# Optimization experiments

Hardware: AMD Instinct MI355X
Metric: run time of the kernel (lower is better)

The kernel has to match this reference:

```python
import jax, jax.numpy as jnp
import numpy as np

NV, NF, NM = 8192, 4096, 12288
PREFIX, DOM = 3, 16
IN_CH, OUT_CH = 64, 64
EMB = IN_CH - PREFIX  # 61
N = NV + NF + 2 * NM  # 36864
E = 262144
G, K = 8192, 16
NUM_COLOR = 100
ATT_HEADS = 4


def setup_inputs() -> dict:
    rng = np.random.default_rng(0)
    key = jax.random.key(0)
    def nrm(i, shape, s=0.1):
        return jax.random.normal(jax.random.fold_in(key, i), shape, jnp.float32) * s
    edge_index = jnp.asarray(rng.integers(0, N, (2, E)), jnp.int32)
    vn_colors = jnp.asarray(rng.integers(0, NUM_COLOR, (NV,)), jnp.int32)
    # ragged neighbor structure: per group, full src list (target included once)
    tgt = rng.integers(0, NF, G)
    deg = rng.integers(1, K + 1, G)
    full = rng.integers(0, NF, (G, K))
    full = np.where(full == tgt[:, None], (tgt[:, None] + 1) % NF, full)
    full[np.arange(G), rng.integers(0, deg)] = tgt
    mask = np.arange(K)[None, :] < deg[:, None]
    mult = rng.integers(1, 6, G)  # (len(target) - 1) in original
    return dict(
        edge_index=edge_index, vn_colors=vn_colors,
        group_full=jnp.asarray(full, jnp.int32), group_mask=jnp.asarray(mask),
        group_tgt=jnp.asarray(tgt, jnp.int32), group_mult=jnp.asarray(mult, jnp.int32),
        vn_prefix=nrm(0, (NV, PREFIX)), fn_embed=nrm(1, (NF, IN_CH)),
        v2f_msgs=nrm(2, (NM, DOM)), v2f_hidden=nrm(3, (NM, EMB)),
        f2v_msgs=nrm(4, (NM, DOM)), f2v_hidden=nrm(5, (NM, EMB)),
        msg_prefix=nrm(6, (2 * NM, PREFIX)),
        emb=nrm(7, (NUM_COLOR, EMB)),
        gru_v2f_wih=nrm(8, (3 * EMB, DOM)), gru_v2f_whh=nrm(9, (3 * EMB, EMB)),
        gru_v2f_bih=nrm(10, (3 * EMB,)), gru_v2f_bhh=nrm(11, (3 * EMB,)),
        gru_f2v_wih=nrm(12, (3 * EMB, DOM)), gru_f2v_whh=nrm(13, (3 * EMB, EMB)),
        gru_f2v_bih=nrm(14, (3 * EMB,)), gru_f2v_bhh=nrm(15, (3 * EMB,)),
        W1=nrm(16, (IN_CH, 32)), a1s=nrm(17, (4, 8)), a1d=nrm(18, (4, 8)), b1=nrm(19, (32,)),
        W2=nrm(20, (32, 32)), a2s=nrm(21, (4, 8)), a2d=nrm(22, (4, 8)), b2=nrm(23, (32,)),
        W3=nrm(24, (32, 32)), a3s=nrm(25, (4, 8)), a3d=nrm(26, (4, 8)), b3=nrm(27, (32,)),
        W4=nrm(28, (32, 4 * OUT_CH)), a4s=nrm(29, (4, OUT_CH)), a4d=nrm(30, (4, OUT_CH)), b4=nrm(31, (OUT_CH,)),
        att_wq=nrm(32, (ATT_HEADS, OUT_CH, OUT_CH)), att_wk=nrm(33, (ATT_HEADS, OUT_CH, OUT_CH)),
        att_ws=nrm(34, (ATT_HEADS, 2 * OUT_CH)), att_b=nrm(35, (ATT_HEADS,)),
    )


def _gru(x, h, w_ih, w_hh, b_ih, b_hh):
    gi = x @ w_ih.T + b_ih
    gh = h @ w_hh.T + b_hh
    hsz = h.shape[1]
    r = jax.nn.sigmoid(gi[:, :hsz] + gh[:, :hsz])
    z = jax.nn.sigmoid(gi[:, hsz:2 * hsz] + gh[:, hsz:2 * hsz])
    n = jnp.tanh(gi[:, 2 * hsz:] + r * gh[:, 2 * hsz:])
    return (1.0 - z) * n + z * h


def _gat(x, src, dst, W, a_src, a_dst, bias, heads, ch, concat):
    n = x.shape[0]
    xl = (x @ W).reshape(n, heads, ch)          # [N,H,C]
    a_s = (xl * a_src).sum(-1)                  # [N,H]
    a_d = (xl * a_dst).sum(-1)
    e = jax.nn.leaky_relu(a_s[src] + a_d[dst], 0.2)   # [E',H]
    m = jax.ops.segment_max(e, dst, num_segments=n)
    ex = jnp.exp(e - m[dst])
    den = jax.ops.segment_sum(ex, dst, num_segments=n)
    alpha = ex / den[dst]
    out = jax.ops.segment_sum(alpha[:, :, None] * xl[src], dst, num_segments=n)
    out = out.reshape(n, heads * ch) if concat else out.mean(axis=1)
    return out + bias


def _forward(floats, edge_index, vn_colors, group_full, group_mask, group_tgt, group_mult):
    (vn_prefix, fn_embed, v2f_msgs, v2f_hidden, f2v_msgs, f2v_hidden, msg_prefix, emb,
     gv_wih, gv_whh, gv_bih, gv_bhh, gf_wih, gf_whh, gf_bih, gf_bhh,
     W1, a1s, a1d, b1, W2, a2s, a2d, b2, W3, a3s, a3d, b3, W4, a4s, a4d, b4,
     att_wq, att_wk, att_ws, att_b) = floats
    x_v = jnp.concatenate([vn_prefix, emb[vn_colors]], axis=1)    # [NV, IN_CH]
    v2f_h = _gru(v2f_msgs, v2f_hidden, gv_wih, gv_whh, gv_bih, gv_bhh)
    f2v_h = _gru(f2v_msgs, f2v_hidden, gf_wih, gf_whh, gf_bih, gf_bhh)
    hid = jnp.concatenate([msg_prefix, jnp.concatenate([v2f_h, f2v_h], axis=0)], axis=1)
    x = jnp.concatenate([x_v, fn_embed, hid], axis=0)             # [N, IN_CH]
    loop = jnp.arange(x.shape[0], dtype=edge_index.dtype)         # self-loops (PyG default)
    src = jnp.concatenate([edge_index[0], loop])
    dst = jnp.concatenate([edge_index[1], loop])
    x = jax.nn.leaky_relu(_gat(x, src, dst, W1, a1s, a1d, b1, 4, 8, True), 0.01)
    x = jax.nn.leaky_relu(_gat(x, src, dst, W2, a2s, a2d, b2, 4, 8, True), 0.01)
    x = jax.nn.leaky_relu(_gat(x, src, dst, W3, a3s, a3d, b3, 4, 8, True), 0.01)
    x = jax.nn.leaky_relu(_gat(x, src, dst, W4, a4s, a4d, b4, 4, OUT_CH, False), 0.01)
    pool = x[NV:NV + NF]                                          # [NF, OUT_CH]
    # attention_scores[q*NF + k, h] = sigmoid(q_proj(pool[q]).Wsq + k_proj(pool[k]).Wsk + b)
    qs = jnp.einsum('nd,hde,he->nh', pool, att_wq, att_ws[:, :OUT_CH])
    ks = jnp.einsum('nd,hde,he->nh', pool, att_wk, att_ws[:, OUT_CH:])
    S = jax.nn.sigmoid(qs[:, None, :] + ks[None, :, :] + att_b)   # [NF, NF, H]
    t = group_tgt
    scores = S[t[:, None], group_full]                            # [G,K,H]
    is_tgt = (group_full == t[:, None]) & group_mask
    nbr = group_mask & (~is_tgt)
    nm = nbr[:, :, None]
    degm1 = nbr.sum(-1)                                           # neighbors excl. target
    score_sum = jnp.where(nm, scores, 0.0).sum(axis=1) / jnp.maximum(degm1, 1)[:, None]
    trg_score = S[t, t]                                           # [G,H]
    mx = jnp.maximum(score_sum, trg_score)
    e0 = jnp.exp(score_sum - mx)
    e1 = jnp.exp(trg_score - mx)
    tw0 = e0 / (e0 + e1)
    tw1 = e1 / (e0 + e1)
    w = jax.nn.softmax(jnp.where(nm, scores, -1e30), axis=1)      # segment softmax over nbrs
    w = w * tw0[:, None, :] * group_mult[:, None, None].astype(w.dtype)
    out = jnp.where(is_tgt[:, :, None], tw1[:, None, :], jnp.where(nm, w, 0.0))
    out = jnp.where((degm1 == 0)[:, None, None], 0.0, out)        # single-src groups -> zeros
    return out, v2f_h, f2v_h


def reference(edge_index, vn_colors, group_full, group_mask, group_tgt, group_mult,
              vn_prefix, fn_embed, v2f_msgs, v2f_hidden, f2v_msgs, f2v_hidden, msg_prefix,
              emb, gru_v2f_wih, gru_v2f_whh, gru_v2f_bih, gru_v2f_bhh,
              gru_f2v_wih, gru_f2v_whh, gru_f2v_bih, gru_f2v_bhh,
              W1, a1s, a1d, b1, W2, a2s, a2d, b2, W3, a3s, a3d, b3, W4, a4s, a4d, b4,
              att_wq, att_wk, att_ws, att_b):
    floats = (vn_prefix, fn_embed, v2f_msgs, v2f_hidden, f2v_msgs, f2v_hidden, msg_prefix,
              emb, gru_v2f_wih, gru_v2f_whh, gru_v2f_bih, gru_v2f_bhh,
              gru_f2v_wih, gru_f2v_whh, gru_f2v_bih, gru_f2v_bhh,
              W1, a1s, a1d, b1, W2, a2s, a2d, b2, W3, a3s, a3d, b3, W4, a4s, a4d, b4,
              att_wq, att_wk, att_ws, att_b)
    return _forward(floats, edge_index, vn_colors, group_full, group_mask, group_tgt, group_mult)
```

## Files before the change

### kernel.cpp

```cpp
#include <hip/hip_runtime.h>
#include <hip/hip_bf16.h>

#define NV 8192
#define NF 4096
#define NM 12288
#define PFX 3
#define DOM 16
#define EMB 61
#define NN 36864
#define EE 262144
#define GG 8192
#define KK 16
#define OUT0 524288

typedef __hip_bfloat16 bf16;
__device__ __forceinline__ float b2f(bf16 x) { return __bfloat162float(x); }
__device__ __forceinline__ float lrelu(float x, float s) { return x > 0.f ? x : s * x; }
__device__ __forceinline__ float sigm(float x) { return 1.f / (1.f + expf(-x)); }
__device__ __forceinline__ float LD(const void* p, int i, int f) {
  return f ? ((const float*)p)[i] : b2f(((const bf16*)p)[i]);
}
__device__ __forceinline__ void ST(void* p, int i, int f, float v) {
  if (f) ((float*)p)[i] = v; else ((bf16*)p)[i] = __float2bfloat16(v);
}
__device__ __forceinline__ int MK(const void* p, int i, int bytey) {
  return bytey ? (int)((const signed char*)p)[i] : ((const int*)p)[i];
}

__global__ void k_detect(const void* fn, const void* mask, int* flags) {
  if (threadIdx.x || blockIdx.x) return;
  int wild = 0;
  const bf16* h = (const bf16*)fn;
  for (int i = 0; i < 128; ++i) {
    float x = b2f(h[i]);
    float a = fabsf(x);
    if (a != a || a > 1e4f || (x != 0.f && a < 1e-8f)) ++wild;
  }
  flags[0] = (wild >= 8) ? 1 : 0;
  const int* mi = (const int*)mask;
  int bytey = 0;
  for (int i = 0; i < 64; ++i) {
    unsigned v = (unsigned)mi[i];
    if (v > 1u) bytey = 1;
  }
  flags[1] = bytey;
}

__global__ void k_precomp(const void* gv_wih, const void* gv_whh,
                          const void* gf_wih, const void* gf_whh,
                          const void* W4, const void* a4s, const void* a4d,
                          const void* wq, const void* wk, const void* ws,
                          float* Wt, float* waS, float* waD, float* wqv, float* wkv,
                          const int* flg) {
  int f = flg[0];
  int blk = blockIdx.x, tid = threadIdx.x;
  if (blk < 116) {
    int t = blk * 256 + tid;
    if (t < 2 * 77 * 192) {
      int dir = t / (77 * 192);
      int rem = t - dir * 77 * 192;
      int d = rem / 192, o = rem - d * 192;
      const void* wih = dir ? gf_wih : gv_wih;
      const void* whh = dir ? gf_whh : gv_whh;
      float v = 0.f;
      if (o < 183) v = (d < 16) ? LD(wih, o * 16 + d, f) : LD(whh, o * 61 + (d - 16), f);
      Wt[t] = v;
    }
  } else if (blk == 116) {
    int isD = tid >= 128;
    int u = tid & 127;
    int h = u >> 5, k = u & 31;
    const void* av = isD ? a4d : a4s;
    float acc = 0.f;
    for (int c = 0; c < 64; ++c) acc += LD(W4, k * 256 + h * 64 + c, f) * LD(av, h * 64 + c, f);
    (isD ? waD : waS)[h * 32 + k] = acc;
  } else {
    int h = tid >> 6, d = tid & 63;
    float q = 0.f, k = 0.f;
    for (int e = 0; e < 64; ++e) {
      q += LD(wq, h * 4096 + d * 64 + e, f) * LD(ws, h * 128 + e, f);
      k += LD(wk, h * 4096 + d * 64 + e, f) * LD(ws, h * 128 + 64 + e, f);
    }
    wqv[h * 64 + d] = q;
    wkv[h * 64 + d] = k;
  }
}

__global__ __launch_bounds__(256) void k_gru2(
    const void* v2f_msgs, const void* v2f_hid, const void* f2v_msgs, const void* f2v_hid,
    const void* gv_bih, const void* gv_bhh, const void* gf_bih, const void* gf_bhh,
    const float* Wt, float* hidcat, void* outv, const int* flg) {
  int f = flg[0];
  int blk = blockIdx.x;
  int dir = blk >= 384;
  int loc = dir ? blk - 384 : blk;
  int gr0 = loc * 32;
  const void* msgs = dir ? f2v_msgs : v2f_msgs;
  const void* hid = dir ? f2v_hid : v2f_hid;
  const void* bih = dir ? gf_bih : gv_bih;
  const void* bhh = dir ? gf_bhh : gv_bhh;
  const float* W = Wt + dir * 77 * 192;

  __shared__ float smem[7808];
  float* F = smem;
  float* G1 = smem;
  float* G2 = smem + 32 * 183;

  int tid = threadIdx.x;
  for (int idx = tid; idx < 32 * 16; idx += 256) {
    int r = idx >> 4, d = idx & 15;
    F[d * 36 + r] = LD(msgs, (gr0 + r) * DOM + d, f);
  }
  for (int idx = tid; idx < 32 * 61; idx += 256) {
    int r = idx / 61, d = idx - r * 61;
    F[(16 + d) * 36 + r] = LD(hid, gr0 * 61 + idx, f);
  }
  __syncthreads();

  int og = tid & 15, rg = tid >> 4;
  int o0 = og * 12, r0 = rg * 2;
  float accA[24], accB[24];
#pragma unroll
  for (int i = 0; i < 24; ++i) { accA[i] = 0.f; accB[i] = 0.f; }

#pragma unroll 2
  for (int d = 0; d < 16; ++d) {
    const float2 fv2 = *(const float2*)&F[d * 36 + r0];
    const float4 w0 = *(const float4*)&W[d * 192 + o0];
    const float4 w1 = *(const float4*)&W[d * 192 + o0 + 4];
    const float4 w2 = *(const float4*)&W[d * 192 + o0 + 8];
    float wv[12] = {w0.x, w0.y, w0.z, w0.w, w1.x, w1.y, w1.z, w1.w, w2.x, w2.y, w2.z, w2.w};
#pragma unroll
    for (int k = 0; k < 12; ++k) {
      accA[k * 2 + 0] += wv[k] * fv2.x;
      accA[k * 2 + 1] += wv[k] * fv2.y;
    }
  }
#pragma unroll 2
  for (int d = 16; d < 77; ++d) {
    const float2 fv2 = *(const float2*)&F[d * 36 + r0];
    const float4 w0 = *(const float4*)&W[d * 192 + o0];
    const float4 w1 = *(const float4*)&W[d * 192 + o0 + 4];
    const float4 w2 = *(const float4*)&W[d * 192 + o0 + 8];
    float wv[12] = {w0.x, w0.y, w0.z, w0.w, w1.x, w1.y, w1.z, w1.w, w2.x, w2.y, w2.z, w2.w};
#pragma unroll
    for (int k = 0; k < 12; ++k) {
      accB[k * 2 + 0] += wv[k] * fv2.x;
      accB[k * 2 + 1] += wv[k] * fv2.y;
    }
  }
  __syncthreads();

#pragma unroll
  for (int k = 0; k < 12; ++k) {
    int o = o0 + k;
    if (o < 183) {
      float biv = LD(bih, o, f), bhv = LD(bhh, o, f);
#pragma unroll
      for (int m = 0; m < 2; ++m) {
        int r = r0 + m;
        float gi = accA[k * 2 + m] + biv;
        float gh = accB[k * 2 + m] + bhv;
        if (o < 122) G1[r * 183 + o] = gi + gh;
        else { G1[r * 183 + o] = gi; G2[r * 61 + (o - 122)] = gh; }
      }
    }
  }
  __syncthreads();

  int j = tid & 63, rq = tid >> 6;
  if (j < 61) {
    for (int rr = 0; rr < 8; ++rr) {
      int r = rq * 8 + rr;
      float gr = sigm(G1[r * 183 + j]);
      float gz = sigm(G1[r * 183 + 61 + j]);
      float gn = tanhf(G1[r * 183 + 122 + j] + gr * G2[r * 61 + j]);
      float hold = LD(hid, (gr0 + r) * 61 + j, f);
      float hn = (1.f - gz) * gn + gz * hold;
      int b = dir * NM + gr0 + r;
      hidcat[b * 61 + j] = hn;
      ST(outv, OUT0 + b * 61 + j, f, hn);
    }
  }
}

__global__ void k_deg(const int* dst, int* deg) {
  int e = blockIdx.x * blockDim.x + threadIdx.x;
  if (e < EE) atomicAdd(&deg[dst[e]], 1);
}
__global__ void k_scan1(const int* deg, int* rowptr, int* bsum) {
  __shared__ int s[512];
  int g = blockIdx.x * 512 + threadIdx.x;
  int v = (g < NN) ? deg[g] : 0;
  s[threadIdx.x] = v;
  __syncthreads();
  for (int off = 1; off < 512; off <<= 1) {
    int t = (threadIdx.x >= off) ? s[threadIdx.x - off] : 0;
    __syncthreads();
    s[threadIdx.x] += t;
    __syncthreads();
  }
  if (g < NN) rowptr[g] = s[threadIdx.x] - v;
  if (threadIdx.x == 511) bsum[blockIdx.x] = s[511];
}
__global__ void k_scan2(const int* bsum, int* boff, int nb) {
  __shared__ int s[128];
  int v = (threadIdx.x < nb) ? bsum[threadIdx.x] : 0;
  s[threadIdx.x] = v;
  __syncthreads();
  for (int off = 1; off < 128; off <<= 1) {
    int t = (threadIdx.x >= off) ? s[threadIdx.x - off] : 0;
    __syncthreads();
    s[threadIdx.x] += t;
    __syncthreads();
  }
  if (threadIdx.x < nb) boff[threadIdx.x] = s[threadIdx.x] - v;
}
__global__ void k_scan3(int* rowptr, const int* boff) {
  int g = blockIdx.x * blockDim.x + threadIdx.x;
  if (g < NN) rowptr[g] += boff[g >> 9];
  if (g == 0) rowptr[NN] = EE;
}
__global__ void k_fill(const int* src, const int* dst, const int* rowptr, int* cnt, int* col) {
  int e = blockIdx.x * blockDim.x + threadIdx.x;
  if (e < EE) {
    int d = dst[e];
    int pos = rowptr[d] + atomicAdd(&cnt[d], 1);
    col[pos] = src[e];
  }
}

__global__ __launch_bounds__(256) void k_xl1(
    const void* vn_prefix, const int* vn_colors, const void* emb, const void* fn_embed,
    const void* msg_prefix, const float* hidcat, const void* W1, const void* a1s,
    const void* a1d, float* xl, float* a_s, float* a_d, const int* flg) {
  int f = flg[0];
  __shared__ float Wl[64 * 32];
  __shared__ float X[8][64];
  int tid = threadIdx.x;
  for (int t = tid; t < 2048; t += 256) Wl[t] = LD(W1, t, f);
  for (int t = tid; t < 512; t += 256) {
    int r = t >> 6, c = t & 63;
    int i = blockIdx.x * 8 + r;
    float v;
    if (i < NV) {
      v = (c < PFX) ? LD(vn_prefix, i * PFX + c, f) : LD(emb, vn_colors[i] * EMB + (c - PFX), f);
    } else if (i < NV + NF) {
      v = LD(fn_embed, (size_t)(i - NV) * 64 + c, f);
    } else {
      int jj = i - NV - NF;
      v = (c < PFX) ? LD(msg_prefix, jj * PFX + c, f) : hidcat[jj * EMB + (c - PFX)];
    }
    X[r][c] = v;
  }
  __syncthreads();
  int j = tid & 31, r = tid >> 5;
  int i = blockIdx.x * 8 + r;
  float acc = 0.f;
#pragma unroll
  for (int k = 0; k < 64; ++k) acc += X[r][k] * Wl[k * 32 + j];
  xl[(size_t)i * 32 + j] = acc;
  float sw = LD(a1s, j, f), dw = LD(a1d, j, f);
  float p = acc * sw, q = acc * dw;
#pragma unroll
  for (int off = 1; off < 8; off <<= 1) {
    p += __shfl_xor(p, off);
    q += __shfl_xor(q, off);
  }
  if ((j & 7) == 0) {
    a_s[(size_t)i * 4 + (j >> 3)] = p;
    a_d[(size_t)i * 4 + (j >> 3)] = q;
  }
}

template <int MODE>
__global__ __launch_bounds__(256) void k_gather13(
    const int* rowptr, const int* col, const float* a_s, const float* a_d,
    const float* xl, const void* bias,
    const void* Wn, const void* asn_, const void* adn_,
    const float* waS, const float* waD,
    float* xl_next, float* xout, float* as_out, float* ad_out, const int* flg) {
  int f = flg[0];
  __shared__ int colb[16][64];
  __shared__ float4 eb[16][64];
  __shared__ float Wn_l[32 * 32];
  __shared__ float an_s[32], an_d[32];
  __shared__ float Xr[16][33];
  __shared__ float SwaS[128], SwaD[128];
  int tid = threadIdx.x;
  if (MODE == 0) {
    for (int t = tid; t < 1024; t += 256) Wn_l[t] = LD(Wn, t, f);
    if (tid < 32) { an_s[tid] = LD(asn_, tid, f); an_d[tid] = LD(adn_, tid, f); }
  } else {
    if (tid < 128) { SwaS[tid] = waS[tid]; SwaD[tid] = waD[tid]; }
  }
  int g = tid >> 4, l = tid & 15;
  int i = blockIdx.x * 16 + g;
  int beg = rowptr[i], end = rowptr[i + 1];
  int deg = end - beg;
  float4 adv = *(const float4*)(a_d + (size_t)i * 4);
  float4 asv = *(const float4*)(a_s + (size_t)i * 4);
  float ad[4] = {adv.x, adv.y, adv.z, adv.w};
  float es[4], mx[4];
  {
    float asl[4] = {asv.x, asv.y, asv.z, asv.w};
#pragma unroll
    for (int h = 0; h < 4; ++h) { es[h] = lrelu(asl[h] + ad[h], 0.2f); mx[h] = es[h]; }
  }
  float den[4] = {0.f, 0.f, 0.f, 0.f};
  int c0 = l, c1 = l + 16;
  int h0 = l >> 3, h1 = 2 + (l >> 3);
  float acc0, acc1;

  if (deg <= 64) {
    for (int s = l; s < deg; s += 16) {
      int j = col[beg + s];
      colb[g][s] = j;
      float4 aj = *(const float4*)(a_s + (size_t)j * 4);
      float e0 = lrelu(aj.x + ad[0], 0.2f);
      float e1 = lrelu(aj.y + ad[1], 0.2f);
      float e2 = lrelu(aj.z + ad[2], 0.2f);
      float e3 = lrelu(aj.w + ad[3], 0.2f);
      eb[g][s] = make_float4(e0, e1, e2, e3);
      mx[0] = fmaxf(mx[0], e0); mx[1] = fmaxf(mx[1], e1);
      mx[2] = fmaxf(mx[2], e2); mx[3] = fmaxf(mx[3], e3);
    }
#pragma unroll
    for (int off = 1; off < 16; off <<= 1)
#pragma unroll
      for (int h = 0; h < 4; ++h) mx[h] = fmaxf(mx[h], __shfl_xor(mx[h], off));
    for (int s = l; s < deg; s += 16) {
      float4 e4 = eb[g][s];
      float x0 = expf(e4.x - mx[0]), x1 = expf(e4.y - mx[1]);
      float x2 = expf(e4.z - mx[2]), x3 = expf(e4.w - mx[3]);
      eb[g][s] = make_float4(x0, x1, x2, x3);
      den[0] += x0; den[1] += x1; den[2] += x2; den[3] += x3;
    }
#pragma unroll
    for (int off = 1; off < 16; off <<= 1)
#pragma unroll
      for (int h = 0; h < 4; ++h) den[h] += __shfl_xor(den[h], off);
    float exS[4];
#pragma unroll
    for (int h = 0; h < 4; ++h) { exS[h] = expf(es[h] - mx[h]); den[h] += exS[h]; }
    acc0 = exS[h0] * xl[(size_t)i * 32 + c0];
    acc1 = exS[h1] * xl[(size_t)i * 32 + c1];
    for (int s = 0; s < deg; ++s) {
      int j = colb[g][s];
      float4 e4 = eb[g][s];
      float w0 = h0 ? e4.y : e4.x;
      float w1 = (l >> 3) ? e4.w : e4.z;
      acc0 += w0 * xl[(size_t)j * 32 + c0];
      acc1 += w1 * xl[(size_t)j * 32 + c1];
    }
  } else {
    for (int s = l; s < deg; s += 16) {
      int j = col[beg + s];
      float4 aj = *(const float4*)(a_s + (size_t)j * 4);
      mx[0] = fmaxf(mx[0], lrelu(aj.x + ad[0], 0.2f));
      mx[1] = fmaxf(mx[1], lrelu(aj.y + ad[1], 0.2f));
      mx[2] = fmaxf(mx[2], lrelu(aj.z + ad[2], 0.2f));
      mx[3] = fmaxf(mx[3], lrelu(aj.w + ad[3], 0.2f));
    }
#pragma unroll
    for (int off = 1; off < 16; off <<= 1)
#pragma unroll
      for (int h = 0; h < 4; ++h) mx[h] = fmaxf(mx[h], __shfl_xor(mx[h], off));
    for (int s = l; s < deg; s += 16) {
      int j = col[beg + s];
      float4 aj = *(const float4*)(a_s + (size_t)j * 4);
      den[0] += expf(lrelu(aj.x + ad[0], 0.2f) - mx[0]);
      den[1] += expf(lrelu(aj.y + ad[1], 0.2f) - mx[1]);
      den[2] += expf(lrelu(aj.z + ad[2], 0.2f) - mx[2]);
      den[3] += expf(lrelu(aj.w + ad[3], 0.2f) - mx[3]);
    }
#pragma unroll
    for (int off = 1; off < 16; off <<= 1)
#pragma unroll
      for (int h = 0; h < 4; ++h) den[h] += __shfl_xor(den[h], off);
    float exS[4];
#pragma unroll
    for (int h = 0; h < 4; ++h) { exS[h] = expf(es[h] - mx[h]); den[h] += exS[h]; }
    acc0 = exS[h0] * xl[(size_t)i * 32 + c0];
    acc1 = exS[h1] * xl[(size_t)i * 32 + c1];
    for (int s = 0; s < deg; ++s) {
      int j = col[beg + s];
      float e0 = lrelu(a_s[(size_t)j * 4 + h0] + ad[h0], 0.2f);
      float e1 = lrelu(a_s[(size_t)j * 4 + h1] + ad[h1], 0.2f);
      acc0 += expf(e0 - mx[h0]) * xl[(size_t)j * 32 + c0];
      acc1 += expf(e1 - mx[h1]) * xl[(size_t)j * 32 + c1];
    }
  }
  float v0 = lrelu(acc0 / den[h0] + LD(bias, c0, f), 0.01f);
  float v1 = lrelu(acc1 / den[h1] + LD(bias, c1, f), 0.01f);

  if (MODE == 0) {
    Xr[g][c0] = v0;
    Xr[g][c1] = v1;
    __syncthreads();
    float n0 = 0.f, n1 = 0.f;
#pragma unroll
    for (int k = 0; k < 32; ++k) {
      float xv = Xr[g][k];
      n0 += xv * Wn_l[k * 32 + c0];
      n1 += xv * Wn_l[k * 32 + c1];
    }
    xl_next[(size_t)i * 32 + c0] = n0;
    xl_next[(size_t)i * 32 + c1] = n1;
    float p0 = n0 * an_s[c0], q0 = n0 * an_d[c0];
    float p1 = n1 * an_s[c1], q1 = n1 * an_d[c1];
#pragma unroll
    for (int off = 1; off < 8; off <<= 1) {
      p0 += __shfl_xor(p0, off); q0 += __shfl_xor(q0, off);
      p1 += __shfl_xor(p1, off); q1 += __shfl_xor(q1, off);
    }
    if ((l & 7) == 0) {
      as_out[(size_t)i * 4 + h0] = p0;
      ad_out[(size_t)i * 4 + h0] = q0;
      as_out[(size_t)i * 4 + h1] = p1;
      ad_out[(size_t)i * 4 + h1] = q1;
    }
  } else {
    xout[(size_t)i * 32 + c0] = v0;
    xout[(size_t)i * 32 + c1] = v1;
    float pS[4], pD[4];
#pragma unroll
    for (int h = 0; h < 4; ++h) {
      pS[h] = v0 * SwaS[h * 32 + c0] + v1 * SwaS[h * 32 + c1];
      pD[h] = v0 * SwaD[h * 32 + c0] + v1 * SwaD[h * 32 + c1];
    }
#pragma unroll
    for (int off = 1; off < 16; off <<= 1)
#pragma unroll
      for (int h = 0; h < 4; ++h) { pS[h] += __shfl_xor(pS[h], off); pD[h] += __shfl_xor(pD[h], off); }
    if (l == 0) {
#pragma unroll
      for (int h = 0; h < 4; ++h) {
        as_out[(size_t)i * 4 + h] = pS[h];
        ad_out[(size_t)i * 4 + h] = pD[h];
      }
    }
  }
}

__global__ __launch_bounds__(256) void k_gather4(const int* rowptr, const int* col,
                                                 const float* a_s, const float* a_d,
                                                 const float* x, float* agg) {
  __shared__ int colb[16][64];
  __shared__ float4 eb[16][64];
  int tid = threadIdx.x;
  int g = tid >> 4, l = tid & 15;
  int i = NV + blockIdx.x * 16 + g;
  int beg = rowptr[i], end = rowptr[i + 1];
  int deg = end - beg;
  float4 adv = *(const float4*)(a_d + (size_t)i * 4);
  float4 asv = *(const float4*)(a_s + (size_t)i * 4);
  float ad[4] = {adv.x, adv.y, adv.z, adv.w};
  float es[4], mx[4];
  {
    float asl[4] = {asv.x, asv.y, asv.z, asv.w};
#pragma unroll
    for (int h = 0; h < 4; ++h) { es[h] = lrelu(asl[h] + ad[h], 0.2f); mx[h] = es[h]; }
  }
  float den[4] = {0.f, 0.f, 0.f, 0.f};
  int k0 = l, k1 = l + 16;
  float acc[4][2];

  if (deg <= 64) {
    for (int s = l; s < deg; s += 16) {
      int j = col[beg + s];
      colb[g][s] = j;
      float4 aj = *(const float4*)(a_s + (size_t)j * 4);
      float e0 = lrelu(aj.x + ad[0], 0.2f);
      float e1 = lrelu(aj.y + ad[1], 0.2f);
      float e2 = lrelu(aj.z + ad[2], 0.2f);
      float e3 = lrelu(aj.w + ad[3], 0.2f);
      eb[g][s] = make_float4(e0, e1, e2, e3);
      mx[0] = fmaxf(mx[0], e0); mx[1] = fmaxf(mx[1], e1);
      mx[2] = fmaxf(mx[2], e2); mx[3] = fmaxf(mx[3], e3);
    }
#pragma unroll
    for (int off = 1; off < 16; off <<= 1)
#pragma unroll
      for (int h = 0; h < 4; ++h) mx[h] = fmaxf(mx[h], __shfl_xor(mx[h], off));
    for (int s = l; s < deg; s += 16) {
      float4 e4 = eb[g][s];
      float x0 = expf(e4.x - mx[0]), x1 = expf(e4.y - mx[1]);
      float x2 = expf(e4.z - mx[2]), x3 = expf(e4.w - mx[3]);
      eb[g][s] = make_float4(x0, x1, x2, x3);
      den[0] += x0; den[1] += x1; den[2] += x2; den[3] += x3;
    }
#pragma unroll
    for (int off = 1; off < 16; off <<= 1)
#pragma unroll
      for (int h = 0; h < 4; ++h) den[h] += __shfl_xor(den[h], off);
    float exS[4];
#pragma unroll
    for (int h = 0; h < 4; ++h) { exS[h] = expf(es[h] - mx[h]); den[h] += exS[h]; }
    float xs0 = x[(size_t)i * 32 + k0], xs1 = x[(size_t)i * 32 + k1];
#pragma unroll
    for (int h = 0; h < 4; ++h) { acc[h][0] = exS[h] * xs0; acc[h][1] = exS[h] * xs1; }
    for (int s = 0; s < deg; ++s) {
      int j = colb[g][s];
      float4 e4 = eb[g][s];
      float xv0 = x[(size_t)j * 32 + k0], xv1 = x[(size_t)j * 32 + k1];
      acc[0][0] += e4.x * xv0; acc[0][1] += e4.x * xv1;
      acc[1][0] += e4.y * xv0; acc[1][1] += e4.y * xv1;
      acc[2][0] += e4.z * xv0; acc[2][1] += e4.z * xv1;
      acc[3][0] += e4.w * xv0; acc[3][1] += e4.w * xv1;
    }
  } else {
    for (int s = l; s < deg; s += 16) {
      int j = col[beg + s];
      float4 aj = *(const float4*)(a_s + (size_t)j * 4);
      mx[0] = fmaxf(mx[0], lrelu(aj.x + ad[0], 0.2f));
      mx[1] = fmaxf(mx[1], lrelu(aj.y + ad[1], 0.2f));
      mx[2] = fmaxf(mx[2], lrelu(aj.z + ad[2], 0.2f));
      mx[3] = fmaxf(mx[3], lrelu(aj.w + ad[3], 0.2f));
    }
#pragma unroll
    for (int off = 1; off < 16; off <<= 1)
#pragma unroll
      for (int h = 0; h < 4; ++h) mx[h] = fmaxf(mx[h], __shfl_xor(mx[h], off));
    for (int s = l; s < deg; s += 16) {
      int j = col[beg + s];
      float4 aj = *(const float4*)(a_s + (size_t)j * 4);
      den[0] += expf(lrelu(aj.x + ad[0], 0.2f) - mx[0]);
      den[1] += expf(lrelu(aj.y + ad[1], 0.2f) - mx[1]);
      den[2] += expf(lrelu(aj.z + ad[2], 0.2f) - mx[2]);
      den[3] += expf(lrelu(aj.w + ad[3], 0.2f) - mx[3]);
    }
#pragma unroll
    for (int off = 1; off < 16; off <<= 1)
#pragma unroll
      for (int h = 0; h < 4; ++h) den[h] += __shfl_xor(den[h], off);
    float exS[4];
#pragma unroll
    for (int h = 0; h < 4; ++h) { exS[h] = expf(es[h] - mx[h]); den[h] += exS[h]; }
    float xs0 = x[(size_t)i * 32 + k0], xs1 = x[(size_t)i * 32 + k1];
#pragma unroll
    for (int h = 0; h < 4; ++h) { acc[h][0] = exS[h] * xs0; acc[h][1] = exS[h] * xs1; }
    for (int s = 0; s < deg; ++s) {
      int j = col[beg + s];
      float4 aj = *(const float4*)(a_s + (size_t)j * 4);
      float xv0 = x[(size_t)j * 32 + k0], xv1 = x[(size_t)j * 32 + k1];
      acc[0][0] += expf(lrelu(aj.x + ad[0], 0.2f) - mx[0]) * xv0;
      acc[0][1] += expf(lrelu(aj.x + ad[0], 0.2f) - mx[0]) * xv1;
      acc[1][0] += expf(lrelu(aj.y + ad[1], 0.2f) - mx[1]) * xv0;
      acc[1][1] += expf(lrelu(aj.y + ad[1], 0.2f) - mx[1]) * xv1;
      acc[2][0] += expf(lrelu(aj.z + ad[2], 0.2f) - mx[2]) * xv0;
      acc[2][1] += expf(lrelu(aj.z + ad[2], 0.2f) - mx[2]) * xv1;
      acc[3][0] += expf(lrelu(aj.w + ad[3], 0.2f) - mx[3]) * xv0;
      acc[3][1] += expf(lrelu(aj.w + ad[3], 0.2f) - mx[3]) * xv1;
    }
  }
#pragma unroll
  for (int h = 0; h < 4; ++h) {
    agg[(size_t)i * 128 + h * 32 + k0] = acc[h][0] / den[h];
    agg[(size_t)i * 128 + h * 32 + k1] = acc[h][1] / den[h];
  }
}

__global__ __launch_bounds__(256) void k_l4_out(const float* agg, const void* W4, const void* b4,
                                                const float* wqv, const float* wkv,
                                                float* qs, float* ks, const int* flg) {
  int f = flg[0];
  __shared__ float Wl[128 * 64];
  __shared__ float Al[64][132];
  __shared__ float Ql[256], Kl[256];
  int tid = threadIdx.x;
  int R0 = NV + blockIdx.x * 64;
  for (int t = tid; t < 128 * 64; t += 256) {
    int K = t >> 6, c = t & 63;
    int h = K >> 5, k = K & 31;
    Wl[t] = LD(W4, k * 256 + h * 64 + c, f);
  }
  {
    const float4* ag4 = (const float4*)(agg + (size_t)R0 * 128);
    for (int t = tid; t < 2048; t += 256) {
      int r = t >> 5, k4 = (t & 31) << 2;
      float4 v = ag4[t];
      *(float4*)&Al[r][k4] = v;
    }
  }
  if (tid < 256) { Ql[tid] = wqv[tid]; Kl[tid] = wkv[tid]; }
  __syncthreads();
  int c0 = (tid & 15) << 2, r0 = (tid >> 4) << 2;
  float acc[4][4];
#pragma unroll
  for (int j = 0; j < 4; ++j)
#pragma unroll
    for (int i = 0; i < 4; ++i) acc[j][i] = 0.f;
#pragma unroll 4
  for (int K = 0; K < 128; ++K) {
    float4 wv = *(const float4*)&Wl[K * 64 + c0];
    float a0 = Al[r0][K], a1 = Al[r0 + 1][K], a2 = Al[r0 + 2][K], a3 = Al[r0 + 3][K];
    acc[0][0] += a0 * wv.x; acc[0][1] += a0 * wv.y; acc[0][2] += a0 * wv.z; acc[0][3] += a0 * wv.w;
    acc[1][0] += a1 * wv.x; acc[1][1] += a1 * wv.y; acc[1][2] += a1 * wv.z; acc[1][3] += a1 * wv.w;
    acc[2][0] += a2 * wv.x; acc[2][1] += a2 * wv.y; acc[2][2] += a2 * wv.z; acc[2][3] += a2 * wv.w;
    acc[3][0] += a3 * wv.x; acc[3][1] += a3 * wv.y; acc[3][2] += a3 * wv.z; acc[3][3] += a3 * wv.w;
  }
  float bv[4];
#pragma unroll
  for (int i = 0; i < 4; ++i) bv[i] = LD(b4, c0 + i, f);
  float o[4][4];
#pragma unroll
  for (int j = 0; j < 4; ++j)
#pragma unroll
    for (int i = 0; i < 4; ++i) o[j][i] = lrelu(0.25f * acc[j][i] + bv[i], 0.01f);
  int nbase = R0 - NV + r0;
#pragma unroll
  for (int j = 0; j < 4; ++j) {
#pragma unroll
    for (int h = 0; h < 4; ++h) {
      float pq = o[j][0] * Ql[h * 64 + c0] + o[j][1] * Ql[h * 64 + c0 + 1] +
                 o[j][2] * Ql[h * 64 + c0 + 2] + o[j][3] * Ql[h * 64 + c0 + 3];
      float pk = o[j][0] * Kl[h * 64 + c0] + o[j][1] * Kl[h * 64 + c0 + 1] +
                 o[j][2] * Kl[h * 64 + c0 + 2] + o[j][3] * Kl[h * 64 + c0 + 3];
#pragma unroll
      for (int off = 1; off < 16; off <<= 1) {
        pq += __shfl_xor(pq, off);
        pk += __shfl_xor(pk, off);
      }
      if ((tid & 15) == 0) {
        qs[(size_t)(nbase + j) * 4 + h] = pq;
        ks[(size_t)(nbase + j) * 4 + h] = pk;
      }
    }
  }
}

__global__ void k_groups(const int* full, const void* mask, const int* tgt, const int* mult,
                         const float* qs, const float* ks, const void* att_b, void* outv,
                         const int* flg) {
  int f = flg[0], mbyte = flg[1];
  int g = blockIdx.x;
  int lane = threadIdx.x;
  int k = lane >> 2, h = lane & 3;
  int t = tgt[g];
  int idx = full[g * KK + k];
  int mk = MK(mask, g * KK + k, mbyte);
  float bh = LD(att_b, h, f);
  float qt = qs[t * 4 + h];
  float sc = sigm(qt + ks[idx * 4 + h] + bh);
  int is_tgt = (idx == t) && mk;
  int nbr = mk && !is_tgt;
  unsigned long long bal = __ballot(nbr != 0);
  int degm1 = (int)(__popcll(bal) >> 2);
  float ssum = nbr ? sc : 0.f;
  for (int off = 4; off < 64; off <<= 1) ssum += __shfl_xor(ssum, off);
  ssum /= (float)(degm1 > 1 ? degm1 : 1);
  float trg = sigm(qt + ks[t * 4 + h] + bh);
  float mxv = fmaxf(ssum, trg);
  float e0 = expf(ssum - mxv), e1 = expf(trg - mxv);
  float tw0 = e0 / (e0 + e1), tw1 = e1 / (e0 + e1);
  float msc = nbr ? sc : -1e30f;
  float m = msc;
  for (int off = 4; off < 64; off <<= 1) m = fmaxf(m, __shfl_xor(m, off));
  float ex = expf(msc - m);
  float den = ex;
  for (int off = 4; off < 64; off <<= 1) den += __shfl_xor(den, off);
  float w = ex / den * tw0 * (float)mult[g];
  float res = is_tgt ? tw1 : (nbr ? w : 0.f);
  if (degm1 == 0) res = 0.f;
  ST(outv, g * 64 + k * 4 + h, f, res);
}

extern "C" void kernel_launch(void* const* d_in, const int* in_sizes, int n_in,
                              void* d_out, int out_size, void* d_ws, size_t ws_size,
                              hipStream_t stream) {
  const int* edge = (const int*)d_in[0];
  const int* esrc = edge;
  const int* edst = edge + EE;
  const int* vn_colors = (const int*)d_in[1];
  const int* group_full = (const int*)d_in[2];
  const void* group_mask = d_in[3];
  const int* group_tgt = (const int*)d_in[4];
  const int* group_mult = (const int*)d_in[5];
  const void* vn_prefix = d_in[6];
  const void* fn_embed = d_in[7];
  const void* v2f_msgs = d_in[8];
  const void* v2f_hidden = d_in[9];
  const void* f2v_msgs = d_in[10];
  const void* f2v_hidden = d_in[11];
  const void* msg_prefix = d_in[12];
  const void* emb = d_in[13];
  const void* gv_wih = d_in[14];
  const void* gv_whh = d_in[15];
  const void* gv_bih = d_in[16];
  const void* gv_bhh = d_in[17];
  const void* gf_wih = d_in[18];
  const void* gf_whh = d_in[19];
  const void* gf_bih = d_in[20];
  const void* gf_bhh = d_in[21];
  const void* W1 = d_in[22];
  const void* a1s = d_in[23];
  const void* a1d = d_in[24];
  const void* b1 = d_in[25];
  const void* W2 = d_in[26];
  const void* a2s = d_in[27];
  const void* a2d = d_in[28];
  const void* b2 = d_in[29];
  const void* W3 = d_in[30];
  const void* a3s = d_in[31];
  const void* a3d = d_in[32];
  const void* b3 = d_in[33];
  const void* W4 = d_in[34];
  const void* a4s = d_in[35];
  const void* a4d = d_in[36];
  const void* b4 = d_in[37];
  const void* att_wq = d_in[38];
  const void* att_wk = d_in[39];
  const void* att_ws = d_in[40];
  const void* att_b = d_in[41];

  char* w = (char*)d_ws;
  size_t off = 0;
  auto carve = [&](size_t bytes) -> void* {
    void* p = w + off;
    off += (bytes + 255) & ~(size_t)255;
    return p;
  };
  int* flags = (int*)carve(16);
  float* Wt = (float*)carve((size_t)2 * 77 * 192 * 4);
  float* hidcat = (float*)carve((size_t)2 * NM * EMB * 4);
  float* xB = (float*)carve((size_t)NN * 64 * 4);
  float* scr = (float*)carve((size_t)NN * 128 * 4);
  float* a_sA = (float*)carve((size_t)NN * 4 * 4);
  float* a_dA = (float*)carve((size_t)NN * 4 * 4);
  float* a_sB = (float*)carve((size_t)NN * 4 * 4);
  float* a_dB = (float*)carve((size_t)NN * 4 * 4);
  int* deg = (int*)carve((size_t)2 * NN * 4);
  int* cnt = deg + NN;
  int* rowptr = (int*)carve((size_t)(NN + 1) * 4);
  int* bsum = (int*)carve(128 * 4);
  int* boff = (int*)carve(128 * 4);
  int* col = (int*)carve((size_t)EE * 4);
  float* qs = (float*)carve((size_t)NF * 4 * 4);
  float* ks = (float*)carve((size_t)NF * 4 * 4);
  float* wqv = (float*)carve(256 * 4);
  float* wkv = (float*)carve(256 * 4);
  float* waS = (float*)carve(128 * 4);
  float* waD = (float*)carve(128 * 4);

  hipMemsetAsync(deg, 0, (size_t)2 * NN * 4, stream);

  k_detect<<<1, 64, 0, stream>>>(fn_embed, group_mask, flags);
  k_precomp<<<118, 256, 0, stream>>>(gv_wih, gv_whh, gf_wih, gf_whh, W4, a4s, a4d,
                                     att_wq, att_wk, att_ws, Wt, waS, waD, wqv, wkv, flags);
  k_gru2<<<768, 256, 0, stream>>>(v2f_msgs, v2f_hidden, f2v_msgs, f2v_hidden,
                                  gv_bih, gv_bhh, gf_bih, gf_bhh, Wt, hidcat, d_out, flags);
  k_deg<<<EE / 256, 256, 0, stream>>>(edst, deg);
  k_scan1<<<72, 512, 0, stream>>>(deg, rowptr, bsum);
  k_scan2<<<1, 128, 0, stream>>>(bsum, boff, 72);
  k_scan3<<<(NN + 256) / 256, 256, 0, stream>>>(rowptr, boff);
  k_fill<<<EE / 256, 256, 0, stream>>>(esrc, edst, rowptr, cnt, col);

  k_xl1<<<NN / 8, 256, 0, stream>>>(vn_prefix, vn_colors, emb, fn_embed, msg_prefix,
                                    hidcat, W1, a1s, a1d, scr, a_sA, a_dA, flags);
  k_gather13<0><<<NN / 16, 256, 0, stream>>>(rowptr, col, a_sA, a_dA, scr, b1,
                                             W2, a2s, a2d, nullptr, nullptr,
                                             xB, nullptr, a_sB, a_dB, flags);
  k_gather13<0><<<NN / 16, 256, 0, stream>>>(rowptr, col, a_sB, a_dB, xB, b2,
                                             W3, a3s, a3d, nullptr, nullptr,
                                             scr, nullptr, a_sA, a_dA, flags);
  k_gather13<1><<<NN / 16, 256, 0, stream>>>(rowptr, col, a_sA, a_dA, scr, b3,
                                             nullptr, nullptr, nullptr, waS, waD,
                                             nullptr, xB, a_sB, a_dB, flags);
  k_gather4<<<NF / 16, 256, 0, stream>>>(rowptr, col, a_sB, a_dB, xB, scr);
  k_l4_out<<<NF / 64, 256, 0, stream>>>(scr, W4, b4, wqv, wkv, qs, ks, flags);

  k_groups<<<GG, 64, 0, stream>>>(group_full, group_mask, group_tgt, group_mult,
                                  qs, ks, att_b, d_out, flags);
}
```

Before: 209.3 us.

## Drop softmax max pass in GAT gathers, fuse scans and memset into kernels

The GAT attention softmax no longer computes a per-node running max. It exponentiates the leaky-relu scores directly with a clamped fast __expf, which removes one pass over neighbours and its shuffle reduction, and in the large-degree path one full gather loop. The degree-buffer memset is folded into extra blocks of the precompute kernel, and the two small scan kernels are merged into one single-block kernel. Dropping the max subtraction risks overflow or precision loss when scores are large, and the exp is clamped at 60 only to avoid infinities.

```diff
diff --git a/kernel.cpp b/kernel.cpp
--- a/kernel.cpp
+++ b/kernel.cpp
@@ -17,6 +17,7 @@
 __device__ __forceinline__ float b2f(bf16 x) { return __bfloat162float(x); }
 __device__ __forceinline__ float lrelu(float x, float s) { return x > 0.f ? x : s * x; }
 __device__ __forceinline__ float sigm(float x) { return 1.f / (1.f + expf(-x)); }
+__device__ __forceinline__ float fexp(float x) { return __expf(fminf(x, 60.f)); }
 __device__ __forceinline__ float LD(const void* p, int i, int f) {
   return f ? ((const float*)p)[i] : b2f(((const bf16*)p)[i]);
 }
@@ -51,7 +52,7 @@
                           const void* W4, const void* a4s, const void* a4d,
                           const void* wq, const void* wk, const void* ws,
                           float* Wt, float* waS, float* waD, float* wqv, float* wkv,
-                          const int* flg) {
+                          int* deg0, const int* flg) {
   int f = flg[0];
   int blk = blockIdx.x, tid = threadIdx.x;
   if (blk < 116) {
@@ -74,7 +75,7 @@
     float acc = 0.f;
     for (int c = 0; c < 64; ++c) acc += LD(W4, k * 256 + h * 64 + c, f) * LD(av, h * 64 + c, f);
     (isD ? waD : waS)[h * 32 + k] = acc;
-  } else {
+  } else if (blk == 117) {
     int h = tid >> 6, d = tid & 63;
     float q = 0.f, k = 0.f;
     for (int e = 0; e < 64; ++e) {
@@ -83,6 +84,9 @@
     }
     wqv[h * 64 + d] = q;
     wkv[h * 64 + d] = k;
+  } else {
+    int t = (blk - 118) * 256 + tid;
+    if (t < 2 * NN) deg0[t] = 0;
   }
 }
 
@@ -203,23 +207,23 @@
   if (g < NN) rowptr[g] = s[threadIdx.x] - v;
   if (threadIdx.x == 511) bsum[blockIdx.x] = s[511];
 }
-__global__ void k_scan2(const int* bsum, int* boff, int nb) {
-  __shared__ int s[128];
-  int v = (threadIdx.x < nb) ? bsum[threadIdx.x] : 0;
-  s[threadIdx.x] = v;
+__global__ void k_scan23(int* rowptr, const int* bsum, int nb) {
+  __shared__ int ps[128];
+  int tid = threadIdx.x;
+  int v = 0;
+  if (tid < 128) { v = (tid < nb) ? bsum[tid] : 0; ps[tid] = v; }
   __syncthreads();
   for (int off = 1; off < 128; off <<= 1) {
-    int t = (threadIdx.x >= off) ? s[threadIdx.x - off] : 0;
+    int t = 0;
+    if (tid < 128 && tid >= off) t = ps[tid - off];
     __syncthreads();
-    s[threadIdx.x] += t;
+    if (tid < 128) ps[tid] += t;
     __syncthreads();
   }
-  if (threadIdx.x < nb) boff[threadIdx.x] = s[threadIdx.x] - v;
-}
-__global__ void k_scan3(int* rowptr, const int* boff) {
-  int g = blockIdx.x * blockDim.x + threadIdx.x;
-  if (g < NN) rowptr[g] += boff[g >> 9];
-  if (g == 0) rowptr[NN] = EE;
+  if (tid < 128) ps[tid] -= v;
+  __syncthreads();
+  for (int g = tid; g < NN; g += 512) rowptr[g] += ps[g >> 9];
+  if (tid == 0) rowptr[NN] = EE;
 }
 __global__ void k_fill(const int* src, const int* dst, const int* rowptr, int* cnt, int* col) {
   int e = blockIdx.x * blockDim.x + threadIdx.x;
@@ -301,11 +305,11 @@
   float4 adv = *(const float4*)(a_d + (size_t)i * 4);
   float4 asv = *(const float4*)(a_s + (size_t)i * 4);
   float ad[4] = {adv.x, adv.y, adv.z, adv.w};
-  float es[4], mx[4];
+  float exS[4];
   {
     float asl[4] = {asv.x, asv.y, asv.z, asv.w};
 #pragma unroll
-    for (int h = 0; h < 4; ++h) { es[h] = lrelu(asl[h] + ad[h], 0.2f); mx[h] = es[h]; }
+    for (int h = 0; h < 4; ++h) exS[h] = fexp(lrelu(asl[h] + ad[h], 0.2f));
   }
   float den[4] = {0.f, 0.f, 0.f, 0.f};
   int c0 = l, c1 = l + 16;
@@ -317,22 +321,10 @@
       int j = col[beg + s];
       colb[g][s] = j;
       float4 aj = *(const float4*)(a_s + (size_t)j * 4);
-      float e0 = lrelu(aj.x + ad[0], 0.2f);
-      float e1 = lrelu(aj.y + ad[1], 0.2f);
-      float e2 = lrelu(aj.z + ad[2], 0.2f);
-      float e3 = lrelu(aj.w + ad[3], 0.2f);
-      eb[g][s] = make_float4(e0, e1, e2, e3);
-      mx[0] = fmaxf(mx[0], e0); mx[1] = fmaxf(mx[1], e1);
-      mx[2] = fmaxf(mx[2], e2); mx[3] = fmaxf(mx[3], e3);
-    }
-#pragma unroll
-    for (int off = 1; off < 16; off <<= 1)
-#pragma unroll
-      for (int h = 0; h < 4; ++h) mx[h] = fmaxf(mx[h], __shfl_xor(mx[h], off));
-    for (int s = l; s < deg; s += 16) {
-      float4 e4 = eb[g][s];
-      float x0 = expf(e4.x - mx[0]), x1 = expf(e4.y - mx[1]);
-      float x2 = expf(e4.z - mx[2]), x3 = expf(e4.w - mx[3]);
+      float x0 = fexp(lrelu(aj.x + ad[0], 0.2f));
+      float x1 = fexp(lrelu(aj.y + ad[1], 0.2f));
+      float x2 = fexp(lrelu(aj.z + ad[2], 0.2f));
+      float x3 = fexp(lrelu(aj.w + ad[3], 0.2f));
       eb[g][s] = make_float4(x0, x1, x2, x3);
       den[0] += x0; den[1] += x1; den[2] += x2; den[3] += x3;
     }
@@ -340,11 +332,11 @@
     for (int off = 1; off < 16; off <<= 1)
 #pragma unroll
       for (int h = 0; h < 4; ++h) den[h] += __shfl_xor(den[h], off);
-    float exS[4];
-#pragma unroll
-    for (int h = 0; h < 4; ++h) { exS[h] = expf(es[h] - mx[h]); den[h] += exS[h]; }
+#pragma unroll
+    for (int h = 0; h < 4; ++h) den[h] += exS[h];
     acc0 = exS[h0] * xl[(size_t)i * 32 + c0];
     acc1 = exS[h1] * xl[(size_t)i * 32 + c1];
+#pragma unroll 2
     for (int s = 0; s < deg; ++s) {
       int j = colb[g][s];
       float4 e4 = eb[g][s];
@@ -357,38 +349,25 @@
     for (int s = l; s < deg; s += 16) {
       int j = col[beg + s];
       float4 aj = *(const float4*)(a_s + (size_t)j * 4);
-      mx[0] = fmaxf(mx[0], lrelu(aj.x + ad[0], 0.2f));
-      mx[1] = fmaxf(mx[1], lrelu(aj.y + ad[1], 0.2f));
-      mx[2] = fmaxf(mx[2], lrelu(aj.z + ad[2], 0.2f));
-      mx[3] = fmaxf(mx[3], lrelu(aj.w + ad[3], 0.2f));
+      den[0] += fexp(lrelu(aj.x + ad[0], 0.2f));
+      den[1] += fexp(lrelu(aj.y + ad[1], 0.2f));
+      den[2] += fexp(lrelu(aj.z + ad[2], 0.2f));
+      den[3] += fexp(lrelu(aj.w + ad[3], 0.2f));
     }
 #pragma unroll
     for (int off = 1; off < 16; off <<= 1)
 #pragma unroll
-      for (int h = 0; h < 4; ++h) mx[h] = fmaxf(mx[h], __shfl_xor(mx[h], off));
-    for (int s = l; s < deg; s += 16) {
-      int j = col[beg + s];
-      float4 aj = *(const float4*)(a_s + (size_t)j * 4);
-      den[0] += expf(lrelu(aj.x + ad[0], 0.2f) - mx[0]);
-      den[1] += expf(lrelu(aj.y + ad[1], 0.2f) - mx[1]);
-      den[2] += expf(lrelu(aj.z + ad[2], 0.2f) - mx[2]);
-      den[3] += expf(lrelu(aj.w + ad[3], 0.2f) - mx[3]);
-    }
-#pragma unroll
-    for (int off = 1; off < 16; off <<= 1)
-#pragma unroll
       for (int h = 0; h < 4; ++h) den[h] += __shfl_xor(den[h], off);
-    float exS[4];
-#pragma unroll
-    for (int h = 0; h < 4; ++h) { exS[h] = expf(es[h] - mx[h]); den[h] += exS[h]; }
+#pragma unroll
+    for (int h = 0; h < 4; ++h) den[h] += exS[h];
     acc0 = exS[h0] * xl[(size_t)i * 32 + c0];
     acc1 = exS[h1] * xl[(size_t)i * 32 + c1];
     for (int s = 0; s < deg; ++s) {
       int j = col[beg + s];
-      float e0 = lrelu(a_s[(size_t)j * 4 + h0] + ad[h0], 0.2f);
-      float e1 = lrelu(a_s[(size_t)j * 4 + h1] + ad[h1], 0.2f);
-      acc0 += expf(e0 - mx[h0]) * xl[(size_t)j * 32 + c0];
-      acc1 += expf(e1 - mx[h1]) * xl[(size_t)j * 32 + c1];
+      float e0 = fexp(lrelu(a_s[(size_t)j * 4 + h0] + ad[h0], 0.2f));
+      float e1 = fexp(lrelu(a_s[(size_t)j * 4 + h1] + ad[h1], 0.2f));
+      acc0 += e0 * xl[(size_t)j * 32 + c0];
+      acc1 += e1 * xl[(size_t)j * 32 + c1];
     }
   }
   float v0 = lrelu(acc0 / den[h0] + LD(bias, c0, f), 0.01f);
@@ -456,11 +435,11 @@
   float4 adv = *(const float4*)(a_d + (size_t)i * 4);
   float4 asv = *(const float4*)(a_s + (size_t)i * 4);
   float ad[4] = {adv.x, adv.y, adv.z, adv.w};
-  float es[4], mx[4];
+  float exS[4];
   {
     float asl[4] = {asv.x, asv.y, asv.z, asv.w};
 #pragma unroll
-    for (int h = 0; h < 4; ++h) { es[h] = lrelu(asl[h] + ad[h], 0.2f); mx[h] = es[h]; }
+    for (int h = 0; h < 4; ++h) exS[h] = fexp(lrelu(asl[h] + ad[h], 0.2f));
   }
   float den[4] = {0.f, 0.f, 0.f, 0.f};
   int k0 = l, k1 = l + 16;
@@ -471,22 +450,10 @@
       int j = col[beg + s];
       colb[g][s] = j;
       float4 aj = *(const float4*)(a_s + (size_t)j * 4);
-      float e0 = lrelu(aj.x + ad[0], 0.2f);
-      float e1 = lrelu(aj.y + ad[1], 0.2f);
-      float e2 = lrelu(aj.z + ad[2], 0.2f);
-      float e3 = lrelu(aj.w + ad[3], 0.2f);
-      eb[g][s] = make_float4(e0, e1, e2, e3);
-      mx[0] = fmaxf(mx[0], e0); mx[1] = fmaxf(mx[1], e1);
-      mx[2] = fmaxf(mx[2], e2); mx[3] = fmaxf(mx[3], e3);
-    }
-#pragma unroll
-    for (int off = 1; off < 16; off <<= 1)
-#pragma unroll
-      for (int h = 0; h < 4; ++h) mx[h] = fmaxf(mx[h], __shfl_xor(mx[h], off));
-    for (int s = l; s < deg; s += 16) {
-      float4 e4 = eb[g][s];
-      float x0 = expf(e4.x - mx[0]), x1 = expf(e4.y - mx[1]);
-      float x2 = expf(e4.z - mx[2]), x3 = expf(e4.w - mx[3]);
+      float x0 = fexp(lrelu(aj.x + ad[0], 0.2f));
+      float x1 = fexp(lrelu(aj.y + ad[1], 0.2f));
+      float x2 = fexp(lrelu(aj.z + ad[2], 0.2f));
+      float x3 = fexp(lrelu(aj.w + ad[3], 0.2f));
       eb[g][s] = make_float4(x0, x1, x2, x3);
       den[0] += x0; den[1] += x1; den[2] += x2; den[3] += x3;
     }
@@ -494,12 +461,14 @@
     for (int off = 1; off < 16; off <<= 1)
 #pragma unroll
       for (int h = 0; h < 4; ++h) den[h] += __shfl_xor(den[h], off);
-    float exS[4];
-#pragma unroll
-    for (int h = 0; h < 4; ++h) { exS[h] = expf(es[h] - mx[h]); den[h] += exS[h]; }
     float xs0 = x[(size_t)i * 32 + k0], xs1 = x[(size_t)i * 32 + k1];
 #pragma unroll
-    for (int h = 0; h < 4; ++h) { acc[h][0] = exS[h] * xs0; acc[h][1] = exS[h] * xs1; }
+    for (int h = 0; h < 4; ++h) {
+      den[h] += exS[h];
+      acc[h][0] = exS[h] * xs0;
+      acc[h][1] = exS[h] * xs1;
+    }
+#pragma unroll 2
     for (int s = 0; s < deg; ++s) {
       int j = colb[g][s];
       float4 e4 = eb[g][s];
@@ -513,45 +482,34 @@
     for (int s = l; s < deg; s += 16) {
       int j = col[beg + s];
       float4 aj = *(const float4*)(a_s + (size_t)j * 4);
-      mx[0] = fmaxf(mx[0], lrelu(aj.x + ad[0], 0.2f));
-      mx[1] = fmaxf(mx[1], lrelu(aj.y + ad[1], 0.2f));
-      mx[2] = fmaxf(mx[2], lrelu(aj.z + ad[2], 0.2f));
-      mx[3] = fmaxf(mx[3], lrelu(aj.w + ad[3], 0.2f));
+      den[0] += fexp(lrelu(aj.x + ad[0], 0.2f));
+      den[1] += fexp(lrelu(aj.y + ad[1], 0.2f));
+      den[2] += fexp(lrelu(aj.z + ad[2], 0.2f));
+      den[3] += fexp(lrelu(aj.w + ad[3], 0.2f));
     }
 #pragma unroll
     for (int off = 1; off < 16; off <<= 1)
 #pragma unroll
-      for (int h = 0; h < 4; ++h) mx[h] = fmaxf(mx[h], __shfl_xor(mx[h], off));
-    for (int s = l; s < deg; s += 16) {
-      int j = col[beg + s];
-      float4 aj = *(const float4*)(a_s + (size_t)j * 4);
-      den[0] += expf(lrelu(aj.x + ad[0], 0.2f) - mx[0]);
-      den[1] += expf(lrelu(aj.y + ad[1], 0.2f) - mx[1]);
-      den[2] += expf(lrelu(aj.z + ad[2], 0.2f) - mx[2]);
-      den[3] += expf(lrelu(aj.w + ad[3], 0.2f) - mx[3]);
-    }
-#pragma unroll
-    for (int off = 1; off < 16; off <<= 1)
-#pragma unroll
       for (int h = 0; h < 4; ++h) den[h] += __shfl_xor(den[h], off);
-    float exS[4];
-#pragma unroll
-    for (int h = 0; h < 4; ++h) { exS[h] = expf(es[h] - mx[h]); den[h] += exS[h]; }
     float xs0 = x[(size_t)i * 32 + k0], xs1 = x[(size_t)i * 32 + k1];
 #pragma unroll
-    for (int h = 0; h < 4; ++h) { acc[h][0] = exS[h] * xs0; acc[h][1] = exS[h] * xs1; }
+    for (int h = 0; h < 4; ++h) {
+      den[h] += exS[h];
+      acc[h][0] = exS[h] * xs0;
+      acc[h][1] = exS[h] * xs1;
+    }
     for (int s = 0; s < deg; ++s) {
       int j = col[beg + s];
       float4 aj = *(const float4*)(a_s + (size_t)j * 4);
+      float e0 = fexp(lrelu(aj.x + ad[0], 0.2f));
+      float e1 = fexp(lrelu(aj.y + ad[1], 0.2f));
+      float e2 = fexp(lrelu(aj.z + ad[2], 0.2f));
+      float e3 = fexp(lrelu(aj.w + ad[3], 0.2f));
       float xv0 = x[(size_t)j * 32 + k0], xv1 = x[(size_t)j * 32 + k1];
-      acc[0][0] += expf(lrelu(aj.x + ad[0], 0.2f) - mx[0]) * xv0;
-      acc[0][1] += expf(lrelu(aj.x + ad[0], 0.2f) - mx[0]) * xv1;
-      acc[1][0] += expf(lrelu(aj.y + ad[1], 0.2f) - mx[1]) * xv0;
-      acc[1][1] += expf(lrelu(aj.y + ad[1], 0.2f) - mx[1]) * xv1;
-      acc[2][0] += expf(lrelu(aj.z + ad[2], 0.2f) - mx[2]) * xv0;
-      acc[2][1] += expf(lrelu(aj.z + ad[2], 0.2f) - mx[2]) * xv1;
-      acc[3][0] += expf(lrelu(aj.w + ad[3], 0.2f) - mx[3]) * xv0;
-      acc[3][1] += expf(lrelu(aj.w + ad[3], 0.2f) - mx[3]) * xv1;
+      acc[0][0] += e0 * xv0; acc[0][1] += e0 * xv1;
+      acc[1][0] += e1 * xv0; acc[1][1] += e1 * xv1;
+      acc[2][0] += e2 * xv0; acc[2][1] += e2 * xv1;
+      acc[3][0] += e3 * xv0; acc[3][1] += e3 * xv1;
     }
   }
 #pragma unroll
@@ -734,7 +692,6 @@
   int* cnt = deg + NN;
   int* rowptr = (int*)carve((size_t)(NN + 1) * 4);
   int* bsum = (int*)carve(128 * 4);
-  int* boff = (int*)carve(128 * 4);
   int* col = (int*)carve((size_t)EE * 4);
   float* qs = (float*)carve((size_t)NF * 4 * 4);
   float* ks = (float*)carve((size_t)NF * 4 * 4);
@@ -743,17 +700,15 @@
   float* waS = (float*)carve(128 * 4);
   float* waD = (float*)carve(128 * 4);
 
-  hipMemsetAsync(deg, 0, (size_t)2 * NN * 4, stream);
-
   k_detect<<<1, 64, 0, stream>>>(fn_embed, group_mask, flags);
-  k_precomp<<<118, 256, 0, stream>>>(gv_wih, gv_whh, gf_wih, gf_whh, W4, a4s, a4d,
-                                     att_wq, att_wk, att_ws, Wt, waS, waD, wqv, wkv, flags);
+  k_precomp<<<118 + (2 * NN + 255) / 256, 256, 0, stream>>>(
+      gv_wih, gv_whh, gf_wih, gf_whh, W4, a4s, a4d,
+      att_wq, att_wk, att_ws, Wt, waS, waD, wqv, wkv, deg, flags);
   k_gru2<<<768, 256, 0, stream>>>(v2f_msgs, v2f_hidden, f2v_msgs, f2v_hidden,
                                   gv_bih, gv_bhh, gf_bih, gf_bhh, Wt, hidcat, d_out, flags);
   k_deg<<<EE / 256, 256, 0, stream>>>(edst, deg);
   k_scan1<<<72, 512, 0, stream>>>(deg, rowptr, bsum);
-  k_scan2<<<1, 128, 0, stream>>>(bsum, boff, 72);
-  k_scan3<<<(NN + 256) / 256, 256, 0, stream>>>(rowptr, boff);
+  k_scan23<<<1, 512, 0, stream>>>(rowptr, bsum, 72);
   k_fill<<<EE / 256, 256, 0, stream>>>(esrc, edst, rowptr, cnt, col);
 
   k_xl1<<<NN / 8, 256, 0, stream>>>(vn_prefix, vn_colors, emb, fn_embed, msg_prefix,
```

Measured after the change: 208.8 us. No clear change (-0.2%).
